# Kernel optimization log

Measured on AMD Instinct MI355X. Metric: run time of the kernel, lower is better.

The kernel has to match this reference:

```python
import jax, jax.numpy as jnp
import numpy as np
import itertools

NX = 21      # number of state variables x
ND = 5       # number of drugs
B, T = 128, 2048
K2 = 0.5     # MM2 saturation constant
K3 = 0.5     # Hill saturation constant


def _build_library():
    lin_idx = np.arange(NX, dtype=np.int64)
    drug_idx = np.array(list(itertools.product(range(NX), range(ND))), dtype=np.int64)   # [105,2]
    bilin_idx = np.array(list(itertools.combinations(range(NX), 2)), dtype=np.int64)     # [210,2]
    mm2_idx = bilin_idx.copy()                                                            # [210,2]
    hill_idx = np.arange(NX, dtype=np.int64)
    return lin_idx, drug_idx, bilin_idx, mm2_idx, hill_idx


def setup_inputs() -> dict:
    key = jax.random.key(0)
    k1, k2 = jax.random.split(key)
    lin_idx, drug_idx, bilin_idx, mm2_idx, hill_idx = _build_library()
    n_terms = 1 + len(lin_idx) + len(drug_idx) + len(bilin_idx) + len(mm2_idx) + len(hill_idx)  # 568
    # positive inputs keep Hill/MM2 denominators well-conditioned
    candidates = jax.random.uniform(k1, (B, T, 1 + NX + ND), dtype=jnp.float32)
    a = (jax.random.normal(k2, (n_terms,), dtype=jnp.float32) * 0.1)
    uses_self = jnp.asarray(np.random.default_rng(1).integers(0, 2, n_terms).astype(bool))
    return {
        "candidates": candidates,
        "a": a,
        "lin_idx": jnp.asarray(lin_idx),
        "drug_idx": jnp.asarray(drug_idx),
        "bilin_idx": jnp.asarray(bilin_idx),
        "mm2_idx": jnp.asarray(mm2_idx),
        "hill_idx": jnp.asarray(hill_idx),
        "uses_self": uses_self,
    }


def reference(candidates, a, lin_idx, drug_idx, bilin_idx, mm2_idx, hill_idx, uses_self):
    con = candidates[:, :, 0:1]            # [B,T,1]
    x = candidates[:, :, 1:1 + NX]         # [B,T,21]
    drug = candidates[:, :, 1 + NX:]       # [B,T,5]

    xm = x[:, :, mm2_idx[:, 0]]
    xh = x[:, :, hill_idx]
    terms = jnp.concatenate([
        con,
        x[:, :, lin_idx],
        x[:, :, drug_idx[:, 0]] * drug[:, :, drug_idx[:, 1]],
        x[:, :, bilin_idx[:, 0]] * x[:, :, bilin_idx[:, 1]],
        xm * x[:, :, mm2_idx[:, 1]] / (K2 + xm),
        xh / (K3 + xh),
    ], axis=2)                              # [B,T,568]

    # per-column zeroing: for i >= 2, zero if (uses_self[i] and a[i] > 0) or (not uses_self[i] and a[i] < 0)
    idx = jnp.arange(terms.shape[2])
    zero_col = jnp.where(uses_self, a > 0.0, a < 0.0) & (idx >= 2)
    terms = jnp.where(zero_col[None, None, :], jnp.zeros((), terms.dtype), terms)
    return terms @ a                        # [B,T]
```

## Files before the change

### kernel.cpp

```cpp
#include <hip/hip_runtime.h>

#define NXC 21
#define NDR 5
#define NFEAT 27
#define NTERMS 568
#define OFF_LX 1
#define OFF_LY 22
#define OFF_D  43
#define OFF_BM 148
#define NCOEF  568

__global__ void sindy_prep(const float* __restrict__ a,
                           const int* __restrict__ lin_idx,
                           const int* __restrict__ drug_idx,
                           const int* __restrict__ bilin_idx,
                           const int* __restrict__ mm2_idx,
                           const int* __restrict__ hill_idx,
                           const void* __restrict__ uses_self,
                           float* __restrict__ cfs) {
    __shared__ int s_mode;
    const int tid = threadIdx.x;
    if (tid == 0) {
        int mode = 0;
        const int* u32 = (const int*)uses_self;
        for (int j = 0; j < NTERMS / 4; ++j) {
            int v = u32[j];
            if (v == 0 || v == 1) continue;
            mode = (v == 0x3f800000) ? 2 : 1;
            break;
        }
        s_mode = mode;
    }
    for (int k = tid; k < NCOEF; k += blockDim.x) cfs[k] = 0.f;
    __syncthreads();
    const int mode = s_mode;

    for (int j = tid; j < NTERMS; j += blockDim.x) {
        float av = a[j];
        bool us;
        if (mode == 0)      us = ((const int*)uses_self)[j] != 0;
        else if (mode == 1) us = ((const unsigned char*)uses_self)[j] != 0;
        else                us = ((const float*)uses_self)[j] != 0.f;
        bool zc = (us ? (av > 0.f) : (av < 0.f)) && (j >= 2);
        float ae = zc ? 0.f : av;

        if (j == 0) {
            cfs[0] = ae;
        } else if (j < 22) {
            int k = j - 1;
            cfs[OFF_LX + lin_idx[k]] = ae;
        } else if (j < 127) {
            int k = j - 22;
            int xi = drug_idx[2 * k], dj = drug_idx[2 * k + 1];
            cfs[OFF_D + dj * NXC + xi] = ae;
        } else if (j < 337) {
            int k = j - 127;
            int i0 = bilin_idx[2 * k], i1 = bilin_idx[2 * k + 1];
            int r = 20 * i0 - (i0 * (i0 - 1)) / 2 + (i1 - i0 - 1);
            cfs[OFF_BM + 2 * r] = ae;
        } else if (j < 547) {
            int k = j - 337;
            int i0 = mm2_idx[2 * k], i1 = mm2_idx[2 * k + 1];
            int r = 20 * i0 - (i0 * (i0 - 1)) / 2 + (i1 - i0 - 1);
            cfs[OFF_BM + 2 * r + 1] = ae;
        } else {
            int k = j - 547;
            cfs[OFF_LY + hill_idx[k]] = ae;
        }
    }
}

#define PTS_PER_BLOCK 512
#define LDS_F4 ((PTS_PER_BLOCK * NFEAT) / 4)

__global__ __launch_bounds__(256) void sindy_main(const float* __restrict__ cand,
                                                  const float* __restrict__ cfs,
                                                  float* __restrict__ out) {
    __shared__ float sx[PTS_PER_BLOCK * NFEAT];
    const int tid = threadIdx.x;
    const size_t base = (size_t)blockIdx.x * PTS_PER_BLOCK;

    const float4* g4 = (const float4*)(cand + base * NFEAT);
    float4* s4 = (float4*)sx;
#pragma unroll
    for (int k = 0; k < 14; ++k) {
        int idx = tid + k * 256;
        if (idx < LDS_F4) s4[idx] = g4[idx];
    }
    __syncthreads();

    const float* r0 = sx + tid * NFEAT;
    const float* r1 = sx + (tid + 256) * NFEAT;

    float x0[NXC], y0[NXC], x1[NXC], y1[NXC];
    const float c0 = cfs[0];
    float acc0 = c0 * r0[0];
    float acc1 = c0 * r1[0];

#pragma unroll
    for (int i = 0; i < NXC; ++i) {
        x0[i] = r0[1 + i];
        x1[i] = r1[1 + i];
        y0[i] = x0[i] * __builtin_amdgcn_rcpf(0.5f + x0[i]);
        y1[i] = x1[i] * __builtin_amdgcn_rcpf(0.5f + x1[i]);
        float lx = cfs[OFF_LX + i], ly = cfs[OFF_LY + i];
        acc0 += lx * x0[i] + ly * y0[i];
        acc1 += lx * x1[i] + ly * y1[i];
    }

#pragma unroll
    for (int d = 0; d < NDR; ++d) {
        float s0 = 0.f, s1 = 0.f;
#pragma unroll
        for (int i = 0; i < NXC; ++i) {
            float c = cfs[OFF_D + d * NXC + i];
            s0 += c * x0[i];
            s1 += c * x1[i];
        }
        acc0 += r0[1 + NXC + d] * s0;
        acc1 += r1[1 + NXC + d] * s1;
    }

    int k = 0;
#pragma unroll
    for (int i = 0; i < NXC - 1; ++i) {
        float sB0 = 0.f, sM0 = 0.f, sB1 = 0.f, sM1 = 0.f;
#pragma unroll
        for (int jj = i + 1; jj < NXC; ++jj) {
            float bk = cfs[OFF_BM + 2 * k];
            float mk = cfs[OFF_BM + 2 * k + 1];
            sB0 += bk * x0[jj];
            sM0 += mk * x0[jj];
            sB1 += bk * x1[jj];
            sM1 += mk * x1[jj];
            ++k;
        }
        acc0 += x0[i] * sB0 + y0[i] * sM0;
        acc1 += x1[i] * sB1 + y1[i] * sM1;
    }

    out[base + tid] = acc0;
    out[base + 256 + tid] = acc1;
}

extern "C" void kernel_launch(void* const* d_in, const int* in_sizes, int n_in,
                              void* d_out, int out_size, void* d_ws, size_t ws_size,
                              hipStream_t stream) {
    const float* cand  = (const float*)d_in[0];
    const float* a     = (const float*)d_in[1];
    const int*   lin   = (const int*)d_in[2];
    const int*   drug  = (const int*)d_in[3];
    const int*   bilin = (const int*)d_in[4];
    const int*   mm2   = (const int*)d_in[5];
    const int*   hill  = (const int*)d_in[6];
    const void*  uses  = d_in[7];
    float* out = (float*)d_out;
    float* cfs = (float*)d_ws;

    sindy_prep<<<1, 256, 0, stream>>>(a, lin, drug, bilin, mm2, hill, uses, cfs);

    const int npts = out_size;
    const int nblocks = npts / PTS_PER_BLOCK;
    sindy_main<<<nblocks, 256, 0, stream>>>(cand, cfs, out);
}
```

Before: 101.0 us.

## Fuse coefficient prep into main kernel and load candidates via direct global-to-LDS

Removes the separate single-block prep kernel. Each block now rebuilds the 568 coefficient table in shared memory while its candidate tile streams into LDS through global_load_lds DMA instead of register round-trips. The intent is to drop one kernel launch and the serialized dependency on the prep kernel, and to overlap coefficient setup with the tile load. The cost is redundant coefficient work in every block and extra index-array reads. Coefficient reads in the main loop now come from LDS rather than global/scalar memory. There is also a risk that the global_load_lds writes are not waited on before __syncthreads.

New measurement: 96.15 us. 4.8% less time.

```diff
diff --git a/kernel.cpp b/kernel.cpp
--- a/kernel.cpp
+++ b/kernel.cpp
@@ -10,90 +10,93 @@
 #define OFF_BM 148
 #define NCOEF  568
 
-__global__ void sindy_prep(const float* __restrict__ a,
-                           const int* __restrict__ lin_idx,
-                           const int* __restrict__ drug_idx,
-                           const int* __restrict__ bilin_idx,
-                           const int* __restrict__ mm2_idx,
-                           const int* __restrict__ hill_idx,
-                           const void* __restrict__ uses_self,
-                           float* __restrict__ cfs) {
-    __shared__ int s_mode;
-    const int tid = threadIdx.x;
-    if (tid == 0) {
-        int mode = 0;
-        const int* u32 = (const int*)uses_self;
-        for (int j = 0; j < NTERMS / 4; ++j) {
-            int v = u32[j];
-            if (v == 0 || v == 1) continue;
-            mode = (v == 0x3f800000) ? 2 : 1;
-            break;
-        }
-        s_mode = mode;
-    }
-    for (int k = tid; k < NCOEF; k += blockDim.x) cfs[k] = 0.f;
-    __syncthreads();
-    const int mode = s_mode;
-
-    for (int j = tid; j < NTERMS; j += blockDim.x) {
-        float av = a[j];
-        bool us;
-        if (mode == 0)      us = ((const int*)uses_self)[j] != 0;
-        else if (mode == 1) us = ((const unsigned char*)uses_self)[j] != 0;
-        else                us = ((const float*)uses_self)[j] != 0.f;
-        bool zc = (us ? (av > 0.f) : (av < 0.f)) && (j >= 2);
-        float ae = zc ? 0.f : av;
-
-        if (j == 0) {
-            cfs[0] = ae;
-        } else if (j < 22) {
-            int k = j - 1;
-            cfs[OFF_LX + lin_idx[k]] = ae;
-        } else if (j < 127) {
-            int k = j - 22;
-            int xi = drug_idx[2 * k], dj = drug_idx[2 * k + 1];
-            cfs[OFF_D + dj * NXC + xi] = ae;
-        } else if (j < 337) {
-            int k = j - 127;
-            int i0 = bilin_idx[2 * k], i1 = bilin_idx[2 * k + 1];
-            int r = 20 * i0 - (i0 * (i0 - 1)) / 2 + (i1 - i0 - 1);
-            cfs[OFF_BM + 2 * r] = ae;
-        } else if (j < 547) {
-            int k = j - 337;
-            int i0 = mm2_idx[2 * k], i1 = mm2_idx[2 * k + 1];
-            int r = 20 * i0 - (i0 * (i0 - 1)) / 2 + (i1 - i0 - 1);
-            cfs[OFF_BM + 2 * r + 1] = ae;
-        } else {
-            int k = j - 547;
-            cfs[OFF_LY + hill_idx[k]] = ae;
-        }
-    }
-}
-
 #define PTS_PER_BLOCK 512
 #define LDS_F4 ((PTS_PER_BLOCK * NFEAT) / 4)
 
-__global__ __launch_bounds__(256) void sindy_main(const float* __restrict__ cand,
-                                                  const float* __restrict__ cfs,
-                                                  float* __restrict__ out) {
-    __shared__ float sx[PTS_PER_BLOCK * NFEAT];
+#define GLOBAL_TO_LDS16(gp, lp)                                              \
+    __builtin_amdgcn_global_load_lds(                                        \
+        (const __attribute__((address_space(1))) void*)(gp),                 \
+        (__attribute__((address_space(3))) void*)(lp), 16, 0, 0)
+
+__global__ __launch_bounds__(256) void sindy_fused(
+    const float* __restrict__ cand,
+    const float* __restrict__ a,
+    const int* __restrict__ lin_idx,
+    const int* __restrict__ drug_idx,
+    const int* __restrict__ bilin_idx,
+    const int* __restrict__ mm2_idx,
+    const int* __restrict__ hill_idx,
+    const void* __restrict__ uses_self,
+    float* __restrict__ out)
+{
+    __shared__ __align__(16) float sx[PTS_PER_BLOCK * NFEAT];
+    __shared__ __align__(16) float scf[NCOEF];
+
     const int tid = threadIdx.x;
     const size_t base = (size_t)blockIdx.x * PTS_PER_BLOCK;
 
     const float4* g4 = (const float4*)(cand + base * NFEAT);
     float4* s4 = (float4*)sx;
 #pragma unroll
-    for (int k = 0; k < 14; ++k) {
-        int idx = tid + k * 256;
-        if (idx < LDS_F4) s4[idx] = g4[idx];
+    for (int k = 0; k < 13; ++k) {
+        const int idx = tid + k * 256;
+        GLOBAL_TO_LDS16(g4 + idx, s4 + idx);
     }
+    if (tid < (LDS_F4 - 13 * 256)) {
+        const int idx = tid + 13 * 256;
+        GLOBAL_TO_LDS16(g4 + idx, s4 + idx);
+    }
+
+    const unsigned int* u32 = (const unsigned int*)uses_self;
+    const int lane = tid & 63;
+    bool bad_byte = false;
+#pragma unroll
+    for (int r = 0; r < 3; ++r) {
+        const int j = lane + r * 64;
+        if (j < NTERMS / 4) {
+            const unsigned int v = u32[j];
+            if (v > 1u && v != 0x3f800000u) bad_byte = true;
+        }
+    }
+    const bool bytemode = __any(bad_byte);
+
+    for (int j = tid; j < NTERMS; j += 256) {
+        const float av = a[j];
+        const bool us = bytemode ? (((const unsigned char*)uses_self)[j] != 0)
+                                 : (u32[j] != 0u);
+        const bool zc = (us ? (av > 0.f) : (av < 0.f)) && (j >= 2);
+        const float ae = zc ? 0.f : av;
+        int dst;
+        if (j == 0) {
+            dst = 0;
+        } else if (j < 22) {
+            dst = OFF_LX + lin_idx[j - 1];
+        } else if (j < 127) {
+            const int k = j - 22;
+            dst = OFF_D + drug_idx[2 * k + 1] * NXC + drug_idx[2 * k];
+        } else if (j < 337) {
+            const int k = j - 127;
+            const int i0 = bilin_idx[2 * k], i1 = bilin_idx[2 * k + 1];
+            const int r = 20 * i0 - (i0 * (i0 - 1)) / 2 + (i1 - i0 - 1);
+            dst = OFF_BM + 2 * r;
+        } else if (j < 547) {
+            const int k = j - 337;
+            const int i0 = mm2_idx[2 * k], i1 = mm2_idx[2 * k + 1];
+            const int r = 20 * i0 - (i0 * (i0 - 1)) / 2 + (i1 - i0 - 1);
+            dst = OFF_BM + 2 * r + 1;
+        } else {
+            dst = OFF_LY + hill_idx[j - 547];
+        }
+        scf[dst] = ae;
+    }
+
     __syncthreads();
 
     const float* r0 = sx + tid * NFEAT;
     const float* r1 = sx + (tid + 256) * NFEAT;
 
     float x0[NXC], y0[NXC], x1[NXC], y1[NXC];
-    const float c0 = cfs[0];
+    const float c0 = scf[0];
     float acc0 = c0 * r0[0];
     float acc1 = c0 * r1[0];
 
@@ -103,7 +106,7 @@
         x1[i] = r1[1 + i];
         y0[i] = x0[i] * __builtin_amdgcn_rcpf(0.5f + x0[i]);
         y1[i] = x1[i] * __builtin_amdgcn_rcpf(0.5f + x1[i]);
-        float lx = cfs[OFF_LX + i], ly = cfs[OFF_LY + i];
+        const float lx = scf[OFF_LX + i], ly = scf[OFF_LY + i];
         acc0 += lx * x0[i] + ly * y0[i];
         acc1 += lx * x1[i] + ly * y1[i];
     }
@@ -113,7 +116,7 @@
         float s0 = 0.f, s1 = 0.f;
 #pragma unroll
         for (int i = 0; i < NXC; ++i) {
-            float c = cfs[OFF_D + d * NXC + i];
+            const float c = scf[OFF_D + d * NXC + i];
             s0 += c * x0[i];
             s1 += c * x1[i];
         }
@@ -127,8 +130,8 @@
         float sB0 = 0.f, sM0 = 0.f, sB1 = 0.f, sM1 = 0.f;
 #pragma unroll
         for (int jj = i + 1; jj < NXC; ++jj) {
-            float bk = cfs[OFF_BM + 2 * k];
-            float mk = cfs[OFF_BM + 2 * k + 1];
+            const float bk = scf[OFF_BM + 2 * k];
+            const float mk = scf[OFF_BM + 2 * k + 1];
             sB0 += bk * x0[jj];
             sM0 += mk * x0[jj];
             sB1 += bk * x1[jj];
@@ -146,6 +149,7 @@
 extern "C" void kernel_launch(void* const* d_in, const int* in_sizes, int n_in,
                               void* d_out, int out_size, void* d_ws, size_t ws_size,
                               hipStream_t stream) {
+    (void)in_sizes; (void)n_in; (void)d_ws; (void)ws_size;
     const float* cand  = (const float*)d_in[0];
     const float* a     = (const float*)d_in[1];
     const int*   lin   = (const int*)d_in[2];
@@ -155,11 +159,8 @@
     const int*   hill  = (const int*)d_in[6];
     const void*  uses  = d_in[7];
     float* out = (float*)d_out;
-    float* cfs = (float*)d_ws;
-
-    sindy_prep<<<1, 256, 0, stream>>>(a, lin, drug, bilin, mm2, hill, uses, cfs);
 
     const int npts = out_size;
     const int nblocks = npts / PTS_PER_BLOCK;
-    sindy_main<<<nblocks, 256, 0, stream>>>(cand, cfs, out);
+    sindy_fused<<<nblocks, 256, 0, stream>>>(cand, a, lin, drug, bilin, mm2, hill, uses, out);
 }
```
